# Kernel optimization log

Hardware: AMD Instinct MI355X
Metric: run time of the kernel (lower is better)

Reference implementation:

```python
import jax, jax.numpy as jnp
import numpy as np

B, T, C = 2, 2048, 1024
NH = 16
HD = C // NH
SCALE = 1.0 / np.sqrt(HD).astype(np.float32)


def setup_inputs() -> dict:
    key = jax.random.key(0)
    k1, k2, k3 = jax.random.split(key, 3)
    x = jax.random.normal(k1, (B, T, C), dtype=jnp.float32)
    # torch Linear stores weight (out,in) and computes x @ W^T; we store the
    # transposed (in,out) layout directly, scaled like default init.
    w_qkv = jax.random.normal(k2, (C, 3 * C), dtype=jnp.float32) * (1.0 / np.sqrt(C))
    w_proj = jax.random.normal(k3, (C, C), dtype=jnp.float32) * (1.0 / np.sqrt(C))
    return {"x": x, "w_qkv": w_qkv, "w_proj": w_proj}


def reference(x, w_qkv, w_proj):
    b, t, c = x.shape
    qkv = x @ w_qkv                                  # (b, t, 3c)
    q, k, v = jnp.split(qkv, 3, axis=-1)
    q = q.reshape(b, t, NH, HD)
    k = k.reshape(b, t, NH, HD)
    v = v.reshape(b, t, NH, HD)
    # scores: (b, nh, t, t) — full materialization, faithful to the original
    att = jnp.einsum("bthd,bshd->bhts", q, k) * SCALE
    causal = jnp.tril(jnp.ones((t, t), dtype=bool))  # (t, t)
    neg = jnp.finfo(att.dtype).min
    att = jnp.where(causal[None, None, :, :], att, neg)
    weights = jax.nn.softmax(att, axis=-1)
    y = jnp.einsum("bhts,bshd->bthd", weights, v).reshape(b, t, c)
    y = y @ w_proj
    return y
```

## Files before the change

kernel.cpp:

```cpp
#include <hip/hip_runtime.h>
#include <hip/hip_bf16.h>
#include <stdint.h>

typedef __bf16 bf16x8 __attribute__((ext_vector_type(8)));
typedef float f32x4 __attribute__((ext_vector_type(4)));
typedef unsigned short us4v __attribute__((ext_vector_type(4)));
typedef unsigned short us8v __attribute__((ext_vector_type(8)));

#define B_   2
#define T_   2048
#define C_   1024
#define NH_  16
#define HD_  64

__device__ __forceinline__ unsigned short f2bf(float f) {
  unsigned int u = __builtin_bit_cast(unsigned int, f);
  u += 0x7fffu + ((u >> 16) & 1u);
  return (unsigned short)(u >> 16);
}
__device__ __forceinline__ float bf2f(unsigned short u) {
  unsigned int x = ((unsigned int)u) << 16;
  return __builtin_bit_cast(float, x);
}

__device__ __forceinline__ void gload16(const void* g, void* l) {
  __builtin_amdgcn_global_load_lds(
      (const __attribute__((address_space(1))) unsigned int*)g,
      (__attribute__((address_space(3))) unsigned int*)l, 16, 0, 0);
}

__device__ __forceinline__ f32x4 mfma16(bf16x8 a, bf16x8 b, f32x4 c) {
  return __builtin_amdgcn_mfma_f32_16x16x32_bf16(a, b, c, 0, 0, 0);
}

__global__ __launch_bounds__(256) void cast_x_kernel(const float4* __restrict__ in,
                                                     us4v* __restrict__ out) {
  int i = blockIdx.x * 256 + threadIdx.x;
  float4 f = in[i];
  us4v o; o[0] = f2bf(f.x); o[1] = f2bf(f.y); o[2] = f2bf(f.z); o[3] = f2bf(f.w);
  out[i] = o;
}

__global__ __launch_bounds__(256) void transpose_cast_kernel(const float* __restrict__ w,
                                                             unsigned short* __restrict__ wT,
                                                             int K, int N) {
  __shared__ float tile[32][33];
  int n0 = blockIdx.x * 32, k0 = blockIdx.y * 32;
  int tx = threadIdx.x, ty = threadIdx.y;
  #pragma unroll
  for (int i = 0; i < 4; ++i)
    tile[ty + 8*i][tx] = w[(size_t)(k0 + ty + 8*i) * N + n0 + tx];
  __syncthreads();
  #pragma unroll
  for (int i = 0; i < 4; ++i)
    wT[(size_t)(n0 + ty + 8*i) * K + k0 + tx] = f2bf(tile[tx][ty + 8*i]);
}

__device__ __forceinline__ void gemm_core(const unsigned short* __restrict__ A,
                                          const unsigned short* __restrict__ Bt,
                                          int K, int m0, int n0,
                                          unsigned short* lA, unsigned short* lB,
                                          f32x4 acc[4][4]) {
  const int t = threadIdx.x;
  const int lane = t & 63, w = t >> 6;
  const int wm = w >> 1, wn = w & 1;
  const int g = lane >> 4, r16 = lane & 15;
  #pragma unroll
  for (int i = 0; i < 4; ++i)
    #pragma unroll
    for (int j = 0; j < 4; ++j) acc[i][j] = (f32x4){0.f, 0.f, 0.f, 0.f};

  for (int k0 = 0; k0 < K; k0 += 64) {
    #pragma unroll
    for (int i = 0; i < 4; ++i) {
      int slot = i * 256 + t;
      int r = slot >> 3, p = slot & 7;
      int q = p ^ (r & 7);
      gload16(A  + (size_t)(m0 + r) * K + k0 + q * 8, lA + slot * 8);
      gload16(Bt + (size_t)(n0 + r) * K + k0 + q * 8, lB + slot * 8);
    }
    asm volatile("s_waitcnt vmcnt(0)" ::: "memory");
    __syncthreads();

    bf16x8 af[4][2], bfr[4][2];
    #pragma unroll
    for (int mi = 0; mi < 4; ++mi)
      #pragma unroll
      for (int kk = 0; kk < 2; ++kk) {
        int r = wm * 64 + mi * 16 + r16;
        int ps = (kk * 4 + g) ^ (r & 7);
        af[mi][kk] = *(const bf16x8*)(lA + r * 64 + ps * 8);
      }
    #pragma unroll
    for (int ni = 0; ni < 4; ++ni)
      #pragma unroll
      for (int kk = 0; kk < 2; ++kk) {
        int r = wn * 64 + ni * 16 + r16;
        int ps = (kk * 4 + g) ^ (r & 7);
        bfr[ni][kk] = *(const bf16x8*)(lB + r * 64 + ps * 8);
      }
    #pragma unroll
    for (int mi = 0; mi < 4; ++mi)
      #pragma unroll
      for (int ni = 0; ni < 4; ++ni)
        #pragma unroll
        for (int kk = 0; kk < 2; ++kk)
          acc[mi][ni] = mfma16(af[mi][kk], bfr[ni][kk], acc[mi][ni]);
    __syncthreads();
  }
}

__device__ __forceinline__ int xcd_swz(int flat, int nwg) {
  int cpx = nwg >> 3;
  return (flat & 7) * cpx + (flat >> 3);
}

__global__ __launch_bounds__(256) void gemm_qkv_kernel(const unsigned short* __restrict__ xb,
                                                       const unsigned short* __restrict__ wT,
                                                       unsigned short* __restrict__ qb,
                                                       unsigned short* __restrict__ kb,
                                                       unsigned short* __restrict__ vb) {
  __shared__ unsigned short lA[128 * 64];
  __shared__ unsigned short lB[128 * 64];
  f32x4 acc[4][4];
  const int nbx = 3 * C_ / 128;
  int flat = xcd_swz(blockIdx.y * nbx + blockIdx.x, nbx * ((B_ * T_) / 128));
  const int m0 = (flat / nbx) * 128, n0 = (flat % nbx) * 128;
  gemm_core(xb, wT, C_, m0, n0, lA, lB, acc);
  const int t = threadIdx.x, lane = t & 63, w = t >> 6;
  const int wm = w >> 1, wn = w & 1, g = lane >> 4, r16 = lane & 15;
  #pragma unroll
  for (int mi = 0; mi < 4; ++mi)
    #pragma unroll
    for (int ni = 0; ni < 4; ++ni)
      #pragma unroll
      for (int j = 0; j < 4; ++j) {
        int gm = m0 + wm * 64 + mi * 16 + g * 4 + j;
        int gn = n0 + wn * 64 + ni * 16 + r16;
        int b = gm >> 11, tt = gm & 2047;
        int s = gn >> 10, rem = gn & 1023;
        int h = rem >> 6, d = rem & 63;
        unsigned short val = f2bf(acc[mi][ni][j]);
        size_t idx = ((size_t)(b * NH_ + h) * T_ + tt) * HD_ + d;
        if (s == 0)      qb[idx] = val;
        else if (s == 1) kb[idx] = val;
        else             vb[idx] = val;
      }
}

__global__ __launch_bounds__(256) void gemm_proj_kernel(const unsigned short* __restrict__ ab,
                                                        const unsigned short* __restrict__ wT,
                                                        float* __restrict__ out) {
  __shared__ unsigned short lA[128 * 64];
  __shared__ unsigned short lB[128 * 64];
  f32x4 acc[4][4];
  const int nbx = C_ / 128;
  int flat = xcd_swz(blockIdx.y * nbx + blockIdx.x, nbx * ((B_ * T_) / 128));
  const int m0 = (flat / nbx) * 128, n0 = (flat % nbx) * 128;
  gemm_core(ab, wT, C_, m0, n0, lA, lB, acc);
  const int t = threadIdx.x, lane = t & 63, w = t >> 6;
  const int wm = w >> 1, wn = w & 1, g = lane >> 4, r16 = lane & 15;
  #pragma unroll
  for (int mi = 0; mi < 4; ++mi)
    #pragma unroll
    for (int ni = 0; ni < 4; ++ni)
      #pragma unroll
      for (int j = 0; j < 4; ++j) {
        int gm = m0 + wm * 64 + mi * 16 + g * 4 + j;
        int gn = n0 + wn * 64 + ni * 16 + r16;
        out[(size_t)gm * C_ + gn] = acc[mi][ni][j];
      }
}

__global__ __launch_bounds__(512, 6) void attn_kernel(const unsigned short* __restrict__ qb,
                                                      const unsigned short* __restrict__ kb,
                                                      const unsigned short* __restrict__ vb,
                                                      unsigned short* __restrict__ ao) {
  __shared__ unsigned short LDS[16384];
  const int pairIdx = blockIdx.x, bh = blockIdx.y;
  const int t = threadIdx.x, lane = t & 63, w = t >> 6;
  const int g = lane >> 4, r16 = lane & 15;
  const int ws = w & 3, sel = w >> 2;
  const int qt0 = (sel ? (31 - pairIdx) : pairIdx) * 64;
  const int myNt = (qt0 >> 6) + 1;
  const int ntMax = 32 - pairIdx;

  const unsigned short* Q  = qb + (size_t)bh * (T_ * HD_);
  const unsigned short* Kp = kb + (size_t)bh * (T_ * HD_);
  const unsigned short* Vp = vb + (size_t)bh * (T_ * HD_);

  bf16x8 qf[2];
  {
    int qrow = qt0 + ws * 16 + r16;
    #pragma unroll
    for (int kk = 0; kk < 2; ++kk) {
      us8v raw = *(const us8v*)(Q + (size_t)qrow * HD_ + kk * 32 + g * 8);
      bf16x8 qv;
      #pragma unroll
      for (int j = 0; j < 8; ++j) qv[j] = (__bf16)(bf2f(raw[j]) * 0.125f);
      qf[kk] = qv;
    }
  }

  f32x4 o[4];
  #pragma unroll
  for (int c = 0; c < 4; ++c) o[c] = (f32x4){0.f, 0.f, 0.f, 0.f};
  float mrun = -__builtin_inff(), lrun = 0.f;

  const int kr = t >> 3, kp = (t & 7) ^ (kr & 7);
  const int colp = (lane & 32) | ((lane & 12) << 1) | ((lane >> 2) & 4) | (lane & 3);
  const int cslot = colp >> 3, cwithin = colp & 7;

  gload16(Kp + (size_t)kr * HD_ + kp * 8, LDS + t * 8);
  us8v vrA = *(const us8v*)(Vp + (size_t)lane * HD_ + w * 8);
  us8v vrB;

  for (int it = 0; it < ntMax; ++it) {
    const int cur = it & 1;
    const unsigned short* Kl = LDS + cur * 4096;
    unsigned short* Vt = LDS + 8192 + cur * 4096;

    asm volatile("s_waitcnt vmcnt(0)" ::: "memory");
    {
      us8v vv = cur ? vrB : vrA;
      #pragma unroll
      for (int u = 0; u < 8; ++u) {
        int d = w * 8 + u;
        Vt[d * 64 + ((cslot ^ u) << 3) + cwithin] = vv[u];
      }
    }
    __syncthreads();

    if (it + 1 < ntMax) {
      const int kv0n = (it + 1) * 64;
      gload16(Kp + (size_t)(kv0n + kr) * HD_ + kp * 8, LDS + (cur ^ 1) * 4096 + t * 8);
      us8v nv = *(const us8v*)(Vp + (size_t)(kv0n + lane) * HD_ + w * 8);
      if (cur) vrA = nv; else vrB = nv;
    }

    if (it < myNt) {
      f32x4 s4t[4];
      #pragma unroll
      for (int c = 0; c < 4; ++c) s4t[c] = (f32x4){0.f, 0.f, 0.f, 0.f};
      #pragma unroll
      for (int c = 0; c < 4; ++c)
        #pragma unroll
        for (int kk = 0; kk < 2; ++kk) {
          int r = c * 16 + r16;
          int ps = (kk * 4 + g) ^ (r & 7);
          bf16x8 kf = *(const bf16x8*)(Kl + r * 64 + ps * 8);
          s4t[c] = mfma16(kf, qf[kk], s4t[c]);
        }
      if (it == myNt - 1) {
        int qloc = ws * 16 + r16;
        #pragma unroll
        for (int c = 0; c < 4; ++c)
          #pragma unroll
          for (int j = 0; j < 4; ++j)
            if (c * 16 + g * 4 + j > qloc) s4t[c][j] = -1e30f;
      }
      float mx = -1e30f;
      #pragma unroll
      for (int c = 0; c < 4; ++c)
        #pragma unroll
        for (int j = 0; j < 4; ++j) mx = fmaxf(mx, s4t[c][j]);
      mx = fmaxf(mx, __shfl_xor(mx, 16));
      mx = fmaxf(mx, __shfl_xor(mx, 32));
      float mn = fmaxf(mrun, mx);
      float alpha = __expf(mrun - mn);
      mrun = mn;
      float rs = 0.f;
      #pragma unroll
      for (int c = 0; c < 4; ++c)
        #pragma unroll
        for (int j = 0; j < 4; ++j) {
          float p = __expf(s4t[c][j] - mn);
          s4t[c][j] = p;
          rs += p;
        }
      rs += __shfl_xor(rs, 16);
      rs += __shfl_xor(rs, 32);
      lrun = lrun * alpha + rs;
      #pragma unroll
      for (int c = 0; c < 4; ++c)
        #pragma unroll
        for (int j = 0; j < 4; ++j) o[c][j] *= alpha;

      bf16x8 pf[2];
      #pragma unroll
      for (int kk = 0; kk < 2; ++kk) {
        bf16x8 p;
        #pragma unroll
        for (int j = 0; j < 4; ++j) {
          p[j]     = (__bf16)s4t[2 * kk][j];
          p[4 + j] = (__bf16)s4t[2 * kk + 1][j];
        }
        pf[kk] = p;
      }
      #pragma unroll
      for (int c = 0; c < 4; ++c) {
        int rv = c * 16 + r16;
        #pragma unroll
        for (int kk = 0; kk < 2; ++kk) {
          int slot = (4 * kk + g) ^ (r16 & 7);
          bf16x8 vf = *(const bf16x8*)(Vt + rv * 64 + slot * 8);
          o[c] = mfma16(vf, pf[kk], o[c]);
        }
      }
    }
  }

  const int deadbuf = ntMax & 1;
  unsigned short* ep = (w < 4)
      ? (LDS + deadbuf * 4096 + w * 1024)
      : (LDS + 8192 + deadbuf * 4096 + (w - 4) * 1024);
  float inv = 1.f / lrun;
  #pragma unroll
  for (int c = 0; c < 4; ++c) {
    us4v pk;
    #pragma unroll
    for (int j = 0; j < 4; ++j) pk[j] = f2bf(o[c][j] * inv);
    int slot = (4 * c + g) ^ r16;
    *(us4v*)(ep + r16 * 64 + slot * 4) = pk;
  }
  asm volatile("s_waitcnt lgkmcnt(0)" ::: "memory");
  __builtin_amdgcn_sched_barrier(0);
  {
    int q = lane >> 2, seg = lane & 3;
    us4v a0 = *(const us4v*)(ep + q * 64 + (((seg * 4 + 0) ^ q) & 15) * 4);
    us4v a1 = *(const us4v*)(ep + q * 64 + (((seg * 4 + 1) ^ q) & 15) * 4);
    us4v a2 = *(const us4v*)(ep + q * 64 + (((seg * 4 + 2) ^ q) & 15) * 4);
    us4v a3 = *(const us4v*)(ep + q * 64 + (((seg * 4 + 3) ^ q) & 15) * 4);
    us8v o0 = {a0[0],a0[1],a0[2],a0[3],a1[0],a1[1],a1[2],a1[3]};
    us8v o1 = {a2[0],a2[1],a2[2],a2[3],a3[0],a3[1],a3[2],a3[3]};
    size_t rowg = (size_t)(bh >> 4) * T_ + qt0 + ws * 16 + q;
    int colg = (bh & 15) * 64 + seg * 16;
    *(us8v*)(ao + rowg * C_ + colg)     = o0;
    *(us8v*)(ao + rowg * C_ + colg + 8) = o1;
  }
}

extern "C" void kernel_launch(void* const* d_in, const int* in_sizes, int n_in,
                              void* d_out, int out_size, void* d_ws, size_t ws_size,
                              hipStream_t stream) {
  const float* x      = (const float*)d_in[0];
  const float* w_qkv  = (const float*)d_in[1];
  const float* w_proj = (const float*)d_in[2];
  float* out = (float*)d_out;
  char* ws = (char*)d_ws;

  unsigned short* xb     = (unsigned short*)(ws);
  unsigned short* wqkvT  = (unsigned short*)(ws + 8388608);
  unsigned short* wprojT = (unsigned short*)(ws + 14680064);
  unsigned short* qb     = (unsigned short*)(ws + 16777216);
  unsigned short* kb     = (unsigned short*)(ws + 25165824);
  unsigned short* vb     = (unsigned short*)(ws + 33554432);
  unsigned short* ao     = xb;

  cast_x_kernel<<<4096, 256, 0, stream>>>((const float4*)x, (us4v*)xb);
  transpose_cast_kernel<<<dim3(3 * C_ / 32, C_ / 32), dim3(32, 8), 0, stream>>>(
      w_qkv, wqkvT, C_, 3 * C_);
  transpose_cast_kernel<<<dim3(C_ / 32, C_ / 32), dim3(32, 8), 0, stream>>>(
      w_proj, wprojT, C_, C_);
  gemm_qkv_kernel<<<dim3(3 * C_ / 128, (B_ * T_) / 128), 256, 0, stream>>>(
      xb, wqkvT, qb, kb, vb);
  attn_kernel<<<dim3(16, 32), 512, 0, stream>>>(qb, kb, vb, ao);
  gemm_proj_kernel<<<dim3(C_ / 128, (B_ * T_) / 128), 256, 0, stream>>>(
      ao, wprojT, out);
}
```

Baseline: 131.1 us.

## Load K fragments directly from global into registers, drop K LDS staging

The attention kernel no longer stages K tiles through shared memory. Each wave loads its K MFMA fragments straight from global memory into registers, prefetched one tile ahead, and only V still goes through a halved LDS buffer. The aim is to cut LDS traffic and footprint and to remove the K LDS reads. In exchange it adds redundant global K loads across waves and more registers, so the occupancy hint is lowered from 6 to 4. The epilogue now reuses LDS after an added barrier, and the vmcnt waits are changed to match the new load ordering.

Result: slower. 146.4 us (+11.7%).

```diff
diff --git a/kernel.cpp b/kernel.cpp
--- a/kernel.cpp
+++ b/kernel.cpp
@@ -172,11 +172,11 @@
       }
 }
 
-__global__ __launch_bounds__(512, 6) void attn_kernel(const unsigned short* __restrict__ qb,
+__global__ __launch_bounds__(512, 4) void attn_kernel(const unsigned short* __restrict__ qb,
                                                       const unsigned short* __restrict__ kb,
                                                       const unsigned short* __restrict__ vb,
                                                       unsigned short* __restrict__ ao) {
-  __shared__ unsigned short LDS[16384];
+  __shared__ unsigned short LDS[8192];
   const int pairIdx = blockIdx.x, bh = blockIdx.y;
   const int t = threadIdx.x, lane = t & 63, w = t >> 6;
   const int g = lane >> 4, r16 = lane & 15;
@@ -207,50 +207,54 @@
   for (int c = 0; c < 4; ++c) o[c] = (f32x4){0.f, 0.f, 0.f, 0.f};
   float mrun = -__builtin_inff(), lrun = 0.f;
 
-  const int kr = t >> 3, kp = (t & 7) ^ (kr & 7);
   const int colp = (lane & 32) | ((lane & 12) << 1) | ((lane >> 2) & 4) | (lane & 3);
   const int cslot = colp >> 3, cwithin = colp & 7;
 
-  gload16(Kp + (size_t)kr * HD_ + kp * 8, LDS + t * 8);
-  us8v vrA = *(const us8v*)(Vp + (size_t)lane * HD_ + w * 8);
-  us8v vrB;
+  us8v nv = *(const us8v*)(Vp + (size_t)lane * HD_ + w * 8);
+  bf16x8 kf[4][2];
+  #pragma unroll
+  for (int c = 0; c < 4; ++c)
+    #pragma unroll
+    for (int kk = 0; kk < 2; ++kk)
+      kf[c][kk] = *(const bf16x8*)(Kp + (size_t)(c * 16 + r16) * HD_ + kk * 32 + g * 8);
 
   for (int it = 0; it < ntMax; ++it) {
     const int cur = it & 1;
-    const unsigned short* Kl = LDS + cur * 4096;
-    unsigned short* Vt = LDS + 8192 + cur * 4096;
-
-    asm volatile("s_waitcnt vmcnt(0)" ::: "memory");
-    {
-      us8v vv = cur ? vrB : vrA;
-      #pragma unroll
-      for (int u = 0; u < 8; ++u) {
-        int d = w * 8 + u;
-        Vt[d * 64 + ((cslot ^ u) << 3) + cwithin] = vv[u];
-      }
+    unsigned short* Vt = LDS + cur * 4096;
+
+    if (it < myNt) { asm volatile("s_waitcnt vmcnt(8)" ::: "memory"); }
+    else           { asm volatile("s_waitcnt vmcnt(0)" ::: "memory"); }
+    #pragma unroll
+    for (int u = 0; u < 8; ++u) {
+      int d = w * 8 + u;
+      Vt[d * 64 + ((cslot ^ u) << 3) + cwithin] = nv[u];
     }
     __syncthreads();
 
-    if (it + 1 < ntMax) {
-      const int kv0n = (it + 1) * 64;
-      gload16(Kp + (size_t)(kv0n + kr) * HD_ + kp * 8, LDS + (cur ^ 1) * 4096 + t * 8);
-      us8v nv = *(const us8v*)(Vp + (size_t)(kv0n + lane) * HD_ + w * 8);
-      if (cur) vrA = nv; else vrB = nv;
-    }
-
+    f32x4 s4t[4];
     if (it < myNt) {
-      f32x4 s4t[4];
+      asm volatile("s_waitcnt vmcnt(0)" ::: "memory");
       #pragma unroll
       for (int c = 0; c < 4; ++c) s4t[c] = (f32x4){0.f, 0.f, 0.f, 0.f};
       #pragma unroll
       for (int c = 0; c < 4; ++c)
         #pragma unroll
-        for (int kk = 0; kk < 2; ++kk) {
-          int r = c * 16 + r16;
-          int ps = (kk * 4 + g) ^ (r & 7);
-          bf16x8 kf = *(const bf16x8*)(Kl + r * 64 + ps * 8);
-          s4t[c] = mfma16(kf, qf[kk], s4t[c]);
-        }
+        for (int kk = 0; kk < 2; ++kk)
+          s4t[c] = mfma16(kf[c][kk], qf[kk], s4t[c]);
+    }
+
+    if (it + 1 < ntMax)
+      nv = *(const us8v*)(Vp + (size_t)((it + 1) * 64 + lane) * HD_ + w * 8);
+    if (it + 1 < myNt) {
+      const unsigned short* Kn = Kp + (size_t)(it + 1) * 64 * HD_;
+      #pragma unroll
+      for (int c = 0; c < 4; ++c)
+        #pragma unroll
+        for (int kk = 0; kk < 2; ++kk)
+          kf[c][kk] = *(const bf16x8*)(Kn + (size_t)(c * 16 + r16) * HD_ + kk * 32 + g * 8);
+    }
+
+    if (it < myNt) {
       if (it == myNt - 1) {
         int qloc = ws * 16 + r16;
         #pragma unroll
@@ -310,10 +314,9 @@
     }
   }
 
-  const int deadbuf = ntMax & 1;
-  unsigned short* ep = (w < 4)
-      ? (LDS + deadbuf * 4096 + w * 1024)
-      : (LDS + 8192 + deadbuf * 4096 + (w - 4) * 1024);
+  __syncthreads();
+
+  unsigned short* ep = LDS + w * 1024;
   float inv = 1.f / lrun;
   #pragma unroll
   for (int c = 0; c < 4; ++c) {
```

## Halve attention block to 4 waves, each wave handling 32 query rows

Applied to the files above, without the earlier changes.

The attention kernel now launches 256 threads per block instead of 512. Each wave processes two 16-row query sub-tiles, so every K and V fragment read from LDS feeds two MFMAs, and each thread issues twice as many global loads per KV tile. This cuts LDS read traffic per MFMA and the number of waves syncing on each barrier. The cost is roughly double the accumulator and score registers per wave, plus lower occupancy (launch bounds 256,3).

New measurement: 126.7 us. 1.03x faster.

```diff
diff --git a/kernel.cpp b/kernel.cpp
--- a/kernel.cpp
+++ b/kernel.cpp
@@ -172,48 +172,55 @@
       }
 }
 
-__global__ __launch_bounds__(512, 6) void attn_kernel(const unsigned short* __restrict__ qb,
+__global__ __launch_bounds__(256, 3) void attn_kernel(const unsigned short* __restrict__ qb,
                                                       const unsigned short* __restrict__ kb,
                                                       const unsigned short* __restrict__ vb,
                                                       unsigned short* __restrict__ ao) {
   __shared__ unsigned short LDS[16384];
   const int pairIdx = blockIdx.x, bh = blockIdx.y;
-  const int t = threadIdx.x, lane = t & 63, w = t >> 6;
+  const int t = threadIdx.x, lane = t & 63, w4 = t >> 6;
   const int g = lane >> 4, r16 = lane & 15;
-  const int ws = w & 3, sel = w >> 2;
-  const int qt0 = (sel ? (31 - pairIdx) : pairIdx) * 64;
-  const int myNt = (qt0 >> 6) + 1;
+  const int sel = w4 >> 1, halfsel = w4 & 1;
+  const int tileBase = sel ? (31 - pairIdx) : pairIdx;
+  const int qt0 = tileBase * 64 + halfsel * 32;
+  const int myNt = tileBase + 1;
   const int ntMax = 32 - pairIdx;
 
   const unsigned short* Q  = qb + (size_t)bh * (T_ * HD_);
   const unsigned short* Kp = kb + (size_t)bh * (T_ * HD_);
   const unsigned short* Vp = vb + (size_t)bh * (T_ * HD_);
 
-  bf16x8 qf[2];
-  {
-    int qrow = qt0 + ws * 16 + r16;
+  bf16x8 qf[2][2];
+  #pragma unroll
+  for (int h = 0; h < 2; ++h) {
+    int qrow = qt0 + h * 16 + r16;
     #pragma unroll
     for (int kk = 0; kk < 2; ++kk) {
       us8v raw = *(const us8v*)(Q + (size_t)qrow * HD_ + kk * 32 + g * 8);
       bf16x8 qv;
       #pragma unroll
       for (int j = 0; j < 8; ++j) qv[j] = (__bf16)(bf2f(raw[j]) * 0.125f);
-      qf[kk] = qv;
+      qf[h][kk] = qv;
     }
   }
 
-  f32x4 o[4];
-  #pragma unroll
-  for (int c = 0; c < 4; ++c) o[c] = (f32x4){0.f, 0.f, 0.f, 0.f};
-  float mrun = -__builtin_inff(), lrun = 0.f;
-
-  const int kr = t >> 3, kp = (t & 7) ^ (kr & 7);
+  f32x4 o[2][4];
+  #pragma unroll
+  for (int h = 0; h < 2; ++h)
+    #pragma unroll
+    for (int c = 0; c < 4; ++c) o[h][c] = (f32x4){0.f, 0.f, 0.f, 0.f};
+  float mrun[2] = {-__builtin_inff(), -__builtin_inff()};
+  float lrun[2] = {0.f, 0.f};
+
+  const int kr0 = t >> 3,        kp0 = (t & 7) ^ (kr0 & 7);
+  const int kr1 = (t + 256) >> 3, kp1 = (t & 7) ^ (kr1 & 7);
   const int colp = (lane & 32) | ((lane & 12) << 1) | ((lane >> 2) & 4) | (lane & 3);
   const int cslot = colp >> 3, cwithin = colp & 7;
 
-  gload16(Kp + (size_t)kr * HD_ + kp * 8, LDS + t * 8);
-  us8v vrA = *(const us8v*)(Vp + (size_t)lane * HD_ + w * 8);
-  us8v vrB;
+  gload16(Kp + (size_t)kr0 * HD_ + kp0 * 8, LDS + t * 8);
+  gload16(Kp + (size_t)kr1 * HD_ + kp1 * 8, LDS + (t + 256) * 8);
+  us8v nv0 = *(const us8v*)(Vp + (size_t)lane * HD_ + w4 * 16);
+  us8v nv1 = *(const us8v*)(Vp + (size_t)lane * HD_ + w4 * 16 + 8);
 
   for (int it = 0; it < ntMax; ++it) {
     const int cur = it & 1;
@@ -221,27 +228,33 @@
     unsigned short* Vt = LDS + 8192 + cur * 4096;
 
     asm volatile("s_waitcnt vmcnt(0)" ::: "memory");
-    {
-      us8v vv = cur ? vrB : vrA;
-      #pragma unroll
-      for (int u = 0; u < 8; ++u) {
-        int d = w * 8 + u;
-        Vt[d * 64 + ((cslot ^ u) << 3) + cwithin] = vv[u];
-      }
+    #pragma unroll
+    for (int u = 0; u < 8; ++u) {
+      int d = w4 * 16 + u;
+      Vt[d * 64 + ((cslot ^ u) << 3) + cwithin] = nv0[u];
+    }
+    #pragma unroll
+    for (int u = 0; u < 8; ++u) {
+      int d = w4 * 16 + 8 + u;
+      Vt[d * 64 + ((cslot ^ u) << 3) + cwithin] = nv1[u];
     }
     __syncthreads();
 
     if (it + 1 < ntMax) {
       const int kv0n = (it + 1) * 64;
-      gload16(Kp + (size_t)(kv0n + kr) * HD_ + kp * 8, LDS + (cur ^ 1) * 4096 + t * 8);
-      us8v nv = *(const us8v*)(Vp + (size_t)(kv0n + lane) * HD_ + w * 8);
-      if (cur) vrA = nv; else vrB = nv;
+      unsigned short* Kn = LDS + (cur ^ 1) * 4096;
+      gload16(Kp + (size_t)(kv0n + kr0) * HD_ + kp0 * 8, Kn + t * 8);
+      gload16(Kp + (size_t)(kv0n + kr1) * HD_ + kp1 * 8, Kn + (t + 256) * 8);
+      nv0 = *(const us8v*)(Vp + (size_t)(kv0n + lane) * HD_ + w4 * 16);
+      nv1 = *(const us8v*)(Vp + (size_t)(kv0n + lane) * HD_ + w4 * 16 + 8);
     }
 
     if (it < myNt) {
-      f32x4 s4t[4];
-      #pragma unroll
-      for (int c = 0; c < 4; ++c) s4t[c] = (f32x4){0.f, 0.f, 0.f, 0.f};
+      f32x4 s4t[2][4];
+      #pragma unroll
+      for (int h = 0; h < 2; ++h)
+        #pragma unroll
+        for (int c = 0; c < 4; ++c) s4t[h][c] = (f32x4){0.f, 0.f, 0.f, 0.f};
       #pragma unroll
       for (int c = 0; c < 4; ++c)
         #pragma unroll
@@ -249,53 +262,59 @@
           int r = c * 16 + r16;
           int ps = (kk * 4 + g) ^ (r & 7);
           bf16x8 kf = *(const bf16x8*)(Kl + r * 64 + ps * 8);
-          s4t[c] = mfma16(kf, qf[kk], s4t[c]);
+          s4t[0][c] = mfma16(kf, qf[0][kk], s4t[0][c]);
+          s4t[1][c] = mfma16(kf, qf[1][kk], s4t[1][c]);
         }
       if (it == myNt - 1) {
-        int qloc = ws * 16 + r16;
+        #pragma unroll
+        for (int h = 0; h < 2; ++h) {
+          int qloc = halfsel * 32 + h * 16 + r16;
+          #pragma unroll
+          for (int c = 0; c < 4; ++c)
+            #pragma unroll
+            for (int j = 0; j < 4; ++j)
+              if (c * 16 + g * 4 + j > qloc) s4t[h][c][j] = -1e30f;
+        }
+      }
+      bf16x8 pf[2][2];
+      #pragma unroll
+      for (int h = 0; h < 2; ++h) {
+        float mx = -1e30f;
         #pragma unroll
         for (int c = 0; c < 4; ++c)
           #pragma unroll
-          for (int j = 0; j < 4; ++j)
-            if (c * 16 + g * 4 + j > qloc) s4t[c][j] = -1e30f;
-      }
-      float mx = -1e30f;
-      #pragma unroll
-      for (int c = 0; c < 4; ++c)
-        #pragma unroll
-        for (int j = 0; j < 4; ++j) mx = fmaxf(mx, s4t[c][j]);
-      mx = fmaxf(mx, __shfl_xor(mx, 16));
-      mx = fmaxf(mx, __shfl_xor(mx, 32));
-      float mn = fmaxf(mrun, mx);
-      float alpha = __expf(mrun - mn);
-      mrun = mn;
-      float rs = 0.f;
-      #pragma unroll
-      for (int c = 0; c < 4; ++c)
-        #pragma unroll
-        for (int j = 0; j < 4; ++j) {
-          float p = __expf(s4t[c][j] - mn);
-          s4t[c][j] = p;
-          rs += p;
+          for (int j = 0; j < 4; ++j) mx = fmaxf(mx, s4t[h][c][j]);
+        mx = fmaxf(mx, __shfl_xor(mx, 16));
+        mx = fmaxf(mx, __shfl_xor(mx, 32));
+        float mn = fmaxf(mrun[h], mx);
+        float alpha = __expf(mrun[h] - mn);
+        mrun[h] = mn;
+        float rs = 0.f;
+        #pragma unroll
+        for (int c = 0; c < 4; ++c)
+          #pragma unroll
+          for (int j = 0; j < 4; ++j) {
+            float p = __expf(s4t[h][c][j] - mn);
+            s4t[h][c][j] = p;
+            rs += p;
+          }
+        rs += __shfl_xor(rs, 16);
+        rs += __shfl_xor(rs, 32);
+        lrun[h] = lrun[h] * alpha + rs;
+        #pragma unroll
+        for (int c = 0; c < 4; ++c)
+          #pragma unroll
+          for (int j = 0; j < 4; ++j) o[h][c][j] *= alpha;
+        #pragma unroll
+        for (int kk = 0; kk < 2; ++kk) {
+          bf16x8 p;
+          #pragma unroll
+          for (int j = 0; j < 4; ++j) {
+            p[j]     = (__bf16)s4t[h][2 * kk][j];
+            p[4 + j] = (__bf16)s4t[h][2 * kk + 1][j];
+          }
+          pf[h][kk] = p;
         }
-      rs += __shfl_xor(rs, 16);
-      rs += __shfl_xor(rs, 32);
-      lrun = lrun * alpha + rs;
-      #pragma unroll
-      for (int c = 0; c < 4; ++c)
-        #pragma unroll
-        for (int j = 0; j < 4; ++j) o[c][j] *= alpha;
-
-      bf16x8 pf[2];
-      #pragma unroll
-      for (int kk = 0; kk < 2; ++kk) {
-        bf16x8 p;
-        #pragma unroll
-        for (int j = 0; j < 4; ++j) {
-          p[j]     = (__bf16)s4t[2 * kk][j];
-          p[4 + j] = (__bf16)s4t[2 * kk + 1][j];
-        }
-        pf[kk] = p;
       }
       #pragma unroll
       for (int c = 0; c < 4; ++c) {
@@ -304,39 +323,43 @@
         for (int kk = 0; kk < 2; ++kk) {
           int slot = (4 * kk + g) ^ (r16 & 7);
           bf16x8 vf = *(const bf16x8*)(Vt + rv * 64 + slot * 8);
-          o[c] = mfma16(vf, pf[kk], o[c]);
+          o[0][c] = mfma16(vf, pf[0][kk], o[0][c]);
+          o[1][c] = mfma16(vf, pf[1][kk], o[1][c]);
         }
       }
     }
   }
 
-  const int deadbuf = ntMax & 1;
-  unsigned short* ep = (w < 4)
-      ? (LDS + deadbuf * 4096 + w * 1024)
-      : (LDS + 8192 + deadbuf * 4096 + (w - 4) * 1024);
-  float inv = 1.f / lrun;
-  #pragma unroll
-  for (int c = 0; c < 4; ++c) {
-    us4v pk;
-    #pragma unroll
-    for (int j = 0; j < 4; ++j) pk[j] = f2bf(o[c][j] * inv);
-    int slot = (4 * c + g) ^ r16;
-    *(us4v*)(ep + r16 * 64 + slot * 4) = pk;
-  }
-  asm volatile("s_waitcnt lgkmcnt(0)" ::: "memory");
-  __builtin_amdgcn_sched_barrier(0);
-  {
-    int q = lane >> 2, seg = lane & 3;
-    us4v a0 = *(const us4v*)(ep + q * 64 + (((seg * 4 + 0) ^ q) & 15) * 4);
-    us4v a1 = *(const us4v*)(ep + q * 64 + (((seg * 4 + 1) ^ q) & 15) * 4);
-    us4v a2 = *(const us4v*)(ep + q * 64 + (((seg * 4 + 2) ^ q) & 15) * 4);
-    us4v a3 = *(const us4v*)(ep + q * 64 + (((seg * 4 + 3) ^ q) & 15) * 4);
-    us8v o0 = {a0[0],a0[1],a0[2],a0[3],a1[0],a1[1],a1[2],a1[3]};
-    us8v o1 = {a2[0],a2[1],a2[2],a2[3],a3[0],a3[1],a3[2],a3[3]};
-    size_t rowg = (size_t)(bh >> 4) * T_ + qt0 + ws * 16 + q;
-    int colg = (bh & 15) * 64 + seg * 16;
-    *(us8v*)(ao + rowg * C_ + colg)     = o0;
-    *(us8v*)(ao + rowg * C_ + colg + 8) = o1;
+  const int deadK = ((ntMax - 1) & 1) ^ 1;
+  unsigned short* ep = LDS + deadK * 4096 + w4 * 1024;
+  #pragma unroll
+  for (int h = 0; h < 2; ++h) {
+    float inv = 1.f / lrun[h];
+    #pragma unroll
+    for (int c = 0; c < 4; ++c) {
+      us4v pk;
+      #pragma unroll
+      for (int j = 0; j < 4; ++j) pk[j] = f2bf(o[h][c][j] * inv);
+      int slot = (4 * c + g) ^ r16;
+      *(us4v*)(ep + r16 * 64 + slot * 4) = pk;
+    }
+    asm volatile("s_waitcnt lgkmcnt(0)" ::: "memory");
+    __builtin_amdgcn_sched_barrier(0);
+    {
+      int q = lane >> 2, seg = lane & 3;
+      us4v a0 = *(const us4v*)(ep + q * 64 + (((seg * 4 + 0) ^ q) & 15) * 4);
+      us4v a1 = *(const us4v*)(ep + q * 64 + (((seg * 4 + 1) ^ q) & 15) * 4);
+      us4v a2 = *(const us4v*)(ep + q * 64 + (((seg * 4 + 2) ^ q) & 15) * 4);
+      us4v a3 = *(const us4v*)(ep + q * 64 + (((seg * 4 + 3) ^ q) & 15) * 4);
+      us8v o0 = {a0[0],a0[1],a0[2],a0[3],a1[0],a1[1],a1[2],a1[3]};
+      us8v o1 = {a2[0],a2[1],a2[2],a2[3],a3[0],a3[1],a3[2],a3[3]};
+      size_t rowg = (size_t)(bh >> 4) * T_ + qt0 + h * 16 + q;
+      int colg = (bh & 15) * 64 + seg * 16;
+      *(us8v*)(ao + rowg * C_ + colg)     = o0;
+      *(us8v*)(ao + rowg * C_ + colg + 8) = o1;
+    }
+    asm volatile("s_waitcnt lgkmcnt(0)" ::: "memory");
+    __builtin_amdgcn_sched_barrier(0);
   }
 }
 
@@ -364,7 +387,7 @@
       w_proj, wprojT, C_, C_);
   gemm_qkv_kernel<<<dim3(3 * C_ / 128, (B_ * T_) / 128), 256, 0, stream>>>(
       xb, wqkvT, qb, kb, vb);
-  attn_kernel<<<dim3(16, 32), 512, 0, stream>>>(qb, kb, vb, ao);
+  attn_kernel<<<dim3(16, 32), 256, 0, stream>>>(qb, kb, vb, ao);
   gemm_proj_kernel<<<dim3(C_ / 128, (B_ * T_) / 128), 256, 0, stream>>>(
       ao, wprojT, out);
 }
```

## Split long causal attention tiles across KV halves with a merge pass

Applied to the files above, without the earlier changes.

Replaces the paired-tile 512-thread attention blocks with 256-thread blocks that each handle one 64-row query tile. Query tiles 16-31 are split into two KV ranges (0-15 and 16-tile), and each half writes its partial output plus running max and sum. A new merge kernel combines the two partials with softmax rescaling. The aim is better load balance and more blocks in flight, at the cost of an extra launch, extra partial-output traffic and rounding the partials to bf16 before the merge. Workspace regions that are no longer needed by this point hold the partial outputs.

Result: faster. 123.4 us (-5.9%).

```diff
diff --git a/kernel.cpp b/kernel.cpp
--- a/kernel.cpp
+++ b/kernel.cpp
@@ -172,18 +172,21 @@
       }
 }
 
-__global__ __launch_bounds__(512, 6) void attn_kernel(const unsigned short* __restrict__ qb,
+__global__ __launch_bounds__(256, 4) void attn_kernel(const unsigned short* __restrict__ qb,
                                                       const unsigned short* __restrict__ kb,
                                                       const unsigned short* __restrict__ vb,
-                                                      unsigned short* __restrict__ ao) {
+                                                      unsigned short* __restrict__ ao,
+                                                      unsigned short* __restrict__ partB,
+                                                      float* __restrict__ mlbuf) {
   __shared__ unsigned short LDS[16384];
-  const int pairIdx = blockIdx.x, bh = blockIdx.y;
-  const int t = threadIdx.x, lane = t & 63, w = t >> 6;
+  const int bx = blockIdx.x, bh = blockIdx.y;
+  int tile, kvLo, kvHi, mode;
+  if (bx < 16)      { tile = 16 + bx; kvLo = 0;  kvHi = 16;       mode = 1; }
+  else if (bx < 32) { tile = 47 - bx; kvLo = 16; kvHi = tile + 1; mode = 2; }
+  else              { tile = 47 - bx; kvLo = 0;  kvHi = tile + 1; mode = 0; }
+  const int qt0 = tile * 64;
+  const int t = threadIdx.x, lane = t & 63, w4 = t >> 6;
   const int g = lane >> 4, r16 = lane & 15;
-  const int ws = w & 3, sel = w >> 2;
-  const int qt0 = (sel ? (31 - pairIdx) : pairIdx) * 64;
-  const int myNt = (qt0 >> 6) + 1;
-  const int ntMax = 32 - pairIdx;
 
   const unsigned short* Q  = qb + (size_t)bh * (T_ * HD_);
   const unsigned short* Kp = kb + (size_t)bh * (T_ * HD_);
@@ -191,7 +194,7 @@
 
   bf16x8 qf[2];
   {
-    int qrow = qt0 + ws * 16 + r16;
+    int qrow = qt0 + w4 * 16 + r16;
     #pragma unroll
     for (int kk = 0; kk < 2; ++kk) {
       us8v raw = *(const us8v*)(Q + (size_t)qrow * HD_ + kk * 32 + g * 8);
@@ -207,38 +210,44 @@
   for (int c = 0; c < 4; ++c) o[c] = (f32x4){0.f, 0.f, 0.f, 0.f};
   float mrun = -__builtin_inff(), lrun = 0.f;
 
-  const int kr = t >> 3, kp = (t & 7) ^ (kr & 7);
+  const int kr0 = t >> 3,         kp0 = (t & 7) ^ (kr0 & 7);
+  const int kr1 = (t + 256) >> 3, kp1 = (t & 7) ^ (kr1 & 7);
   const int colp = (lane & 32) | ((lane & 12) << 1) | ((lane >> 2) & 4) | (lane & 3);
   const int cslot = colp >> 3, cwithin = colp & 7;
 
-  gload16(Kp + (size_t)kr * HD_ + kp * 8, LDS + t * 8);
-  us8v vrA = *(const us8v*)(Vp + (size_t)lane * HD_ + w * 8);
-  us8v vrB;
-
-  for (int it = 0; it < ntMax; ++it) {
-    const int cur = it & 1;
+  gload16(Kp + (size_t)(kvLo * 64 + kr0) * HD_ + kp0 * 8, LDS + t * 8);
+  gload16(Kp + (size_t)(kvLo * 64 + kr1) * HD_ + kp1 * 8, LDS + (t + 256) * 8);
+  us8v nv0 = *(const us8v*)(Vp + (size_t)(kvLo * 64 + lane) * HD_ + w4 * 16);
+  us8v nv1 = *(const us8v*)(Vp + (size_t)(kvLo * 64 + lane) * HD_ + w4 * 16 + 8);
+
+  for (int it = kvLo; it < kvHi; ++it) {
+    const int cur = (it - kvLo) & 1;
     const unsigned short* Kl = LDS + cur * 4096;
     unsigned short* Vt = LDS + 8192 + cur * 4096;
 
     asm volatile("s_waitcnt vmcnt(0)" ::: "memory");
+    #pragma unroll
+    for (int u = 0; u < 8; ++u) {
+      int d = w4 * 16 + u;
+      Vt[d * 64 + ((cslot ^ u) << 3) + cwithin] = nv0[u];
+    }
+    #pragma unroll
+    for (int u = 0; u < 8; ++u) {
+      int d = w4 * 16 + 8 + u;
+      Vt[d * 64 + ((cslot ^ u) << 3) + cwithin] = nv1[u];
+    }
+    __syncthreads();
+
+    if (it + 1 < kvHi) {
+      const int kv0n = (it + 1) * 64;
+      unsigned short* Kn = LDS + (cur ^ 1) * 4096;
+      gload16(Kp + (size_t)(kv0n + kr0) * HD_ + kp0 * 8, Kn + t * 8);
+      gload16(Kp + (size_t)(kv0n + kr1) * HD_ + kp1 * 8, Kn + (t + 256) * 8);
+      nv0 = *(const us8v*)(Vp + (size_t)(kv0n + lane) * HD_ + w4 * 16);
+      nv1 = *(const us8v*)(Vp + (size_t)(kv0n + lane) * HD_ + w4 * 16 + 8);
+    }
+
     {
-      us8v vv = cur ? vrB : vrA;
-      #pragma unroll
-      for (int u = 0; u < 8; ++u) {
-        int d = w * 8 + u;
-        Vt[d * 64 + ((cslot ^ u) << 3) + cwithin] = vv[u];
-      }
-    }
-    __syncthreads();
-
-    if (it + 1 < ntMax) {
-      const int kv0n = (it + 1) * 64;
-      gload16(Kp + (size_t)(kv0n + kr) * HD_ + kp * 8, LDS + (cur ^ 1) * 4096 + t * 8);
-      us8v nv = *(const us8v*)(Vp + (size_t)(kv0n + lane) * HD_ + w * 8);
-      if (cur) vrA = nv; else vrB = nv;
-    }
-
-    if (it < myNt) {
       f32x4 s4t[4];
       #pragma unroll
       for (int c = 0; c < 4; ++c) s4t[c] = (f32x4){0.f, 0.f, 0.f, 0.f};
@@ -251,8 +260,8 @@
           bf16x8 kf = *(const bf16x8*)(Kl + r * 64 + ps * 8);
           s4t[c] = mfma16(kf, qf[kk], s4t[c]);
         }
-      if (it == myNt - 1) {
-        int qloc = ws * 16 + r16;
+      if (it == tile) {
+        int qloc = w4 * 16 + r16;
         #pragma unroll
         for (int c = 0; c < 4; ++c)
           #pragma unroll
@@ -310,10 +319,15 @@
     }
   }
 
-  const int deadbuf = ntMax & 1;
-  unsigned short* ep = (w < 4)
-      ? (LDS + deadbuf * 4096 + w * 1024)
-      : (LDS + 8192 + deadbuf * 4096 + (w - 4) * 1024);
+  if (mode && g == 0) {
+    int prow = (bh * 16 + (tile - 16)) * 64 + w4 * 16 + r16;
+    float* mlp = mlbuf + (size_t)prow * 4;
+    if (mode == 1) { mlp[0] = mrun; mlp[1] = lrun; }
+    else           { mlp[2] = mrun; mlp[3] = lrun; }
+  }
+
+  const int deadK = ((kvHi - kvLo - 1) & 1) ^ 1;
+  unsigned short* ep = LDS + deadK * 4096 + w4 * 1024;
   float inv = 1.f / lrun;
   #pragma unroll
   for (int c = 0; c < 4; ++c) {
@@ -333,11 +347,48 @@
     us4v a3 = *(const us4v*)(ep + q * 64 + (((seg * 4 + 3) ^ q) & 15) * 4);
     us8v o0 = {a0[0],a0[1],a0[2],a0[3],a1[0],a1[1],a1[2],a1[3]};
     us8v o1 = {a2[0],a2[1],a2[2],a2[3],a3[0],a3[1],a3[2],a3[3]};
-    size_t rowg = (size_t)(bh >> 4) * T_ + qt0 + ws * 16 + q;
-    int colg = (bh & 15) * 64 + seg * 16;
-    *(us8v*)(ao + rowg * C_ + colg)     = o0;
-    *(us8v*)(ao + rowg * C_ + colg + 8) = o1;
-  }
+    if (mode != 2) {
+      size_t rowg = (size_t)(bh >> 4) * T_ + qt0 + w4 * 16 + q;
+      int colg = (bh & 15) * 64 + seg * 16;
+      *(us8v*)(ao + rowg * C_ + colg)     = o0;
+      *(us8v*)(ao + rowg * C_ + colg + 8) = o1;
+    } else {
+      size_t prow = (size_t)(bh * 16 + (tile - 16)) * 64 + w4 * 16 + q;
+      *(us8v*)(partB + prow * 64 + seg * 16)     = o0;
+      *(us8v*)(partB + prow * 64 + seg * 16 + 8) = o1;
+    }
+  }
+}
+
+__global__ __launch_bounds__(256) void attn_merge_kernel(unsigned short* __restrict__ ao,
+                                                         const unsigned short* __restrict__ partB,
+                                                         const float* __restrict__ mlbuf) {
+  const int blk = blockIdx.x;
+  const int bh = blk >> 4, ti = blk & 15;
+  const int t = threadIdx.x;
+  const int row = t >> 2, seg = t & 3;
+  const size_t prow = (size_t)(bh * 16 + ti) * 64 + row;
+  const float* mlp = mlbuf + prow * 4;
+  float mA = mlp[0], lA = mlp[1], mB = mlp[2], lB = mlp[3];
+  float m = fmaxf(mA, mB);
+  float wA = lA * __expf(mA - m), wB = lB * __expf(mB - m);
+  float rinv = 1.f / (wA + wB);
+  wA *= rinv; wB *= rinv;
+  size_t rowg = (size_t)(bh >> 4) * T_ + (16 + ti) * 64 + row;
+  unsigned short* aop = ao + rowg * C_ + (bh & 15) * 64 + seg * 16;
+  const unsigned short* obp = partB + prow * 64 + seg * 16;
+  us8v oa0 = *(const us8v*)(aop);
+  us8v oa1 = *(const us8v*)(aop + 8);
+  us8v ob0 = *(const us8v*)(obp);
+  us8v ob1 = *(const us8v*)(obp + 8);
+  us8v r0, r1;
+  #pragma unroll
+  for (int j = 0; j < 8; ++j) {
+    r0[j] = f2bf(bf2f(oa0[j]) * wA + bf2f(ob0[j]) * wB);
+    r1[j] = f2bf(bf2f(oa1[j]) * wA + bf2f(ob1[j]) * wB);
+  }
+  *(us8v*)(aop)     = r0;
+  *(us8v*)(aop + 8) = r1;
 }
 
 extern "C" void kernel_launch(void* const* d_in, const int* in_sizes, int n_in,
@@ -356,6 +407,8 @@
   unsigned short* kb     = (unsigned short*)(ws + 25165824);
   unsigned short* vb     = (unsigned short*)(ws + 33554432);
   unsigned short* ao     = xb;
+  unsigned short* partB  = wqkvT;
+  float*          mlbuf  = (float*)(ws + 8388608 + 4194304);
 
   cast_x_kernel<<<4096, 256, 0, stream>>>((const float4*)x, (us4v*)xb);
   transpose_cast_kernel<<<dim3(3 * C_ / 32, C_ / 32), dim3(32, 8), 0, stream>>>(
@@ -364,7 +417,8 @@
       w_proj, wprojT, C_, C_);
   gemm_qkv_kernel<<<dim3(3 * C_ / 128, (B_ * T_) / 128), 256, 0, stream>>>(
       xb, wqkvT, qb, kb, vb);
-  attn_kernel<<<dim3(16, 32), 512, 0, stream>>>(qb, kb, vb, ao);
+  attn_kernel<<<dim3(48, 32), 256, 0, stream>>>(qb, kb, vb, ao, partB, mlbuf);
+  attn_merge_kernel<<<512, 256, 0, stream>>>(ao, partB, mlbuf);
   gemm_proj_kernel<<<dim3(C_ / 128, (B_ * T_) / 128), 256, 0, stream>>>(
       ao, wprojT, out);
 }
```
